# Kernel optimization log

Measured on AMD Instinct MI355X. Metric: run time of the kernel, lower is better.

Reference implementation:

```python
import jax, jax.numpy as jnp
import numpy as np

S_LEN = 256   # seq_len
B = 512       # batch
STATE = 32    # state_dim
ZD = 64       # z_dim
RNN = 512     # rnn_dim
HD = 512      # h_dim
LOG2PI = float(np.log(2.0 * np.pi))


def setup_inputs() -> dict:
    key = jax.random.key(0)
    ks = jax.random.split(key, 12)

    def mat(k, shape, fan_in):
        return jax.random.normal(k, shape, dtype=jnp.float32) * (1.0 / np.sqrt(fan_in))

    z32 = lambda *s: jnp.zeros(s, jnp.float32)
    return {
        "states": jax.random.normal(ks[0], (S_LEN, B, STATE), jnp.float32),
        "z": jax.random.normal(ks[1], (B, ZD), jnp.float32),
        # GRU layer 0: input = concat(state, action) -> 2*STATE
        "Wih0": mat(ks[2], (3 * RNN, 2 * STATE), 2 * STATE),
        "Whh0": mat(ks[3], (3 * RNN, RNN), RNN),
        "bih0": z32(3 * RNN),
        "bhh0": z32(3 * RNN),
        # GRU layer 1: input = hidden of layer 0
        "Wih1": mat(ks[4], (3 * RNN, RNN), RNN),
        "Whh1": mat(ks[5], (3 * RNN, RNN), RNN),
        "bih1": z32(3 * RNN),
        "bhh1": z32(3 * RNN),
        # dec_action_fc: Linear(STATE+ZD+RNN -> HD), ReLU, Linear(HD -> HD), ReLU
        "Wfc1": mat(ks[6], (HD, STATE + ZD + RNN), STATE + ZD + RNN),
        "bfc1": z32(HD),
        "Wfc2": mat(ks[7], (HD, HD), HD),
        "bfc2": z32(HD),
        "Wmean": mat(ks[8], (STATE, HD), HD),
        "bmean": z32(STATE),
        "Wlv": mat(ks[9], (STATE, HD), HD),
        "blv": z32(STATE),
    }


def _gru_step(x, h, Wih, Whh, bih, bhh):
    # PyTorch GRUCell math
    gi = x @ Wih.T + bih  # [B, 3R]
    gh = h @ Whh.T + bhh
    ir, iz, inn = jnp.split(gi, 3, axis=1)
    hr, hz, hn = jnp.split(gh, 3, axis=1)
    r = jax.nn.sigmoid(ir + hr)
    zg = jax.nn.sigmoid(iz + hz)
    n = jnp.tanh(inn + r * hn)
    return (1.0 - zg) * n + zg * h


def reference(states, z, Wih0, Whh0, bih0, bhh0, Wih1, Whh1, bih1, bhh1,
              Wfc1, bfc1, Wfc2, bfc2, Wmean, bmean, Wlv, blv):
    # actions[t] = states[t+1] - states[t]
    actions = states[1:] - states[:-1]
    # loop runs for actions.size(0)-1 = T-2 steps using (states[t], actions[t])
    xs = (states[:-2], actions[:-1])
    Bb = z.shape[0]
    R = Whh0.shape[1]
    h_init = jnp.zeros((2, Bb, R), states.dtype)
    nll_init = jnp.zeros((Bb, states.shape[-1]), states.dtype)

    def step(carry, xt):
        h, nll = carry
        s, a = xt  # [B, STATE] each
        # decode_action: cat(state, z, hidden[-1]) -> MLP -> mean, logvar
        fc_in = jnp.concatenate([s, z, h[1]], axis=1)
        dh = jax.nn.relu(fc_in @ Wfc1.T + bfc1)
        dh = jax.nn.relu(dh @ Wfc2.T + bfc2)
        mean = dh @ Wmean.T + bmean
        logvar = dh @ Wlv.T + blv
        # nll -= Normal(mean, logvar).log_prob(action), std = exp(0.5*logvar)
        nll_t = 0.5 * ((a - mean) ** 2 * jnp.exp(-logvar) + logvar + LOG2PI)
        # update_hidden_state with cat(state, action) through 2-layer GRU
        x_in = jnp.concatenate([s, a], axis=1)
        h0n = _gru_step(x_in, h[0], Wih0, Whh0, bih0, bhh0)
        h1n = _gru_step(h0n, h[1], Wih1, Whh1, bih1, bhh1)
        return (jnp.stack([h0n, h1n]), nll + nll_t), None

    (h, nll), _ = jax.lax.scan(step, (h_init, nll_init), xs)
    return nll  # accumulated NLL, shape [B, STATE]
```

## Files before the change

### kernel.cpp

```cpp
#include <hip/hip_runtime.h>
#include <math.h>

#define BATCH 512
#define LOG2PI 1.8378770664093453f

typedef __attribute__((ext_vector_type(8))) short bfrag;
typedef __attribute__((ext_vector_type(4))) float f32x4;
typedef __attribute__((ext_vector_type(4))) unsigned int u32x4;

#define MFMA(a,b,c) __builtin_amdgcn_mfma_f32_16x16x32_bf16(a,b,c,0,0,0)
#define ASTORE(p,v) __hip_atomic_store((p),(v),__ATOMIC_RELAXED,__HIP_MEMORY_SCOPE_AGENT)
#define ALOAD(p)    __hip_atomic_load((p),__ATOMIC_RELAXED,__HIP_MEMORY_SCOPE_AGENT)

__device__ __forceinline__ void st16_sc1(void* p, u32x4 v){
  asm volatile("global_store_dwordx4 %0, %1, off sc1" :: "v"(p), "v"(v) : "memory");
}

__device__ __forceinline__ float sigm(float x){ return 1.0f/(1.0f+__expf(-x)); }
__device__ __forceinline__ unsigned short f2bf(float f){
  unsigned int u = __builtin_bit_cast(unsigned int, f);
  u += 0x7FFFu + ((u>>16)&1u);
  return (unsigned short)(u>>16);
}
__device__ __forceinline__ bfrag cvt8(const float* __restrict__ p){
  bfrag v;
  #pragma unroll
  for (int e=0;e<8;++e) v[e] = (short)f2bf(p[e]);
  return v;
}
__device__ __forceinline__ bfrag cvt8d(const float* __restrict__ p1, const float* __restrict__ p0){
  bfrag v;
  #pragma unroll
  for (int e=0;e<8;++e) v[e] = (short)f2bf(p1[e]-p0[e]);
  return v;
}

struct Params {
  const float *states, *zin;
  const float *Wih0, *Whh0, *bih0, *bhh0;
  const float *Wih1, *Whh1, *bih1, *bhh1;
  const float *Wfc1, *bfc1, *Wfc2, *bfc2;
  const float *Wmean, *bmean, *Wlv, *blv;
  unsigned short *h0x0, *h0x1, *h0x2;
  unsigned short *h1x0, *h1x1, *h1x2;
  unsigned short *d1x0, *d1x1, *d1x2;
  unsigned short *d2x0, *d2x1, *d2x2;
  float *out;
};

__global__ __launch_bounds__(256, 1) void fused(Params P, unsigned* flags) {
  __shared__ unsigned short sm[74752];
  const int tid  = threadIdx.x;
  const int lane = tid & 63;
  const int wv   = tid >> 6;
  const int r16  = lane & 15, kg = lane >> 4;
  const int blk  = blockIdx.x;
  const int xg   = blk & 7, sub = blk >> 3;

  unsigned short* h0b[3]  = {P.h0x0, P.h0x1, P.h0x2};
  unsigned short* h1b[3]  = {P.h1x0, P.h1x1, P.h1x2};
  unsigned short* dh1b[3] = {P.d1x0, P.d1x1, P.d1x2};
  unsigned short* dh2b[3] = {P.d2x0, P.d2x1, P.d2x2};

  if (xg < 4) {
    const int jt = sub;
    const float* Wsrc[2] = {P.Wih1, P.Whh1};
    #pragma unroll
    for (int m = 0; m < 2; ++m) {
      const float* W = Wsrc[m];
      for (int c = tid; c < 3072; c += 256) {
        int g = c >> 10, rem = c & 1023;
        int r = rem >> 6, k = (rem & 63) << 3;
        *(bfrag*)&sm[(g*16+r)*1032 + m*512 + k] =
          cvt8(&W[((size_t)(g*512 + jt*16 + r))*512 + k]);
      }
    }
  } else if (xg < 6) {
    const int jt = sub;
    for (int c = tid; c < 384; c += 256) {
      int g = c >> 7, rem = c & 127;
      int r = rem >> 3, k = (rem & 7) << 3;
      *(bfrag*)&sm[(g*16+r)*584 + k] =
        cvt8(&P.Wih0[((size_t)(g*512 + jt*16 + r))*64 + k]);
    }
    for (int c = tid; c < 3072; c += 256) {
      int g = c >> 10, rem = c & 1023;
      int r = rem >> 6, k = (rem & 63) << 3;
      *(bfrag*)&sm[(g*16+r)*584 + 64 + k] =
        cvt8(&P.Whh0[((size_t)(g*512 + jt*16 + r))*512 + k]);
    }
  } else if (xg == 6) {
    const int bn = (sub & 7) * 64;
    const int bmB = (sub >> 3) * 128;
    for (int c = tid; c < 4864; c += 256) {
      int n = c / 76, k = (c % 76) << 3;
      *(bfrag*)&sm[n*616 + k] = cvt8(&P.Wfc1[(size_t)(bn + n)*608 + k]);
    }
    for (int c = tid; c < 1024; c += 256) {
      int r = c >> 3, k = (c & 7) << 3;
      *(bfrag*)&sm[47616 + r*64 + k] = cvt8(&P.zin[(size_t)(bmB + r)*64 + k]);
    }
  } else {
    const int bn = (sub & 7) * 64;
    for (int c = tid; c < 4096; c += 256) {
      int n = c >> 6, k = (c & 63) << 3;
      *(bfrag*)&sm[n*520 + k] = cvt8(&P.Wfc2[(size_t)(bn + n)*512 + k]);
    }
    for (int c = tid; c < 4096; c += 256) {
      int m = c >> 6, k = (c & 63) << 3;
      const float* src = (m < 32) ? &P.Wmean[(size_t)m*512 + k]
                                  : &P.Wlv[(size_t)(m-32)*512 + k];
      *(bfrag*)&sm[33280 + m*520 + k] = cvt8(src);
    }
  }

  float b0 = 0.f, b1 = 0.f, b2 = 0.f, b3 = 0.f;
  if (xg < 4) {
    int j = sub*16 + r16;
    b0 = P.bih1[j] + P.bhh1[j];
    b1 = P.bih1[j+512] + P.bhh1[j+512];
    b2 = P.bih1[j+1024]; b3 = P.bhh1[j+1024];
  } else if (xg < 6) {
    int j = sub*16 + r16;
    b0 = P.bih0[j] + P.bhh0[j];
    b1 = P.bih0[j+512] + P.bhh0[j+512];
    b2 = P.bih0[j+1024]; b3 = P.bhh0[j+1024];
  } else if (xg == 6) {
    int nn0 = (sub & 7)*64 + (wv&1)*32 + r16;
    b0 = P.bfc1[nn0]; b1 = P.bfc1[nn0+16];
  } else {
    int nn0 = (sub & 7)*64 + (wv&1)*32 + r16;
    b0 = P.bfc2[nn0]; b1 = P.bfc2[nn0+16];
    int c = wv*16 + r16;
    b2 = (c < 32) ? P.bmean[c] : P.blv[c-32];
  }
  float hs[4][4] = {};
  float nacc0 = 0.f, nacc1 = 0.f;

  for (int u = 0; u <= 256; ++u) {
    if (wv == 0) {
      int pb1 = -1, pb2 = -1;
      const unsigned t1 = (unsigned)u, t2 = (unsigned)(u - 1);
      if (xg >= 4 && xg < 6) {
        if (u >= 1 && lane < 32) pb1 = lane*8 + xg;
        if (u >= 2)              pb2 = (lane>>1)*8 + 2*(xg-4) + (lane&1);
      } else if (xg < 4) {
        if (u >= 1) pb1 = (lane < 32) ? lane*8 + xg : (lane-32)*8 + 4 + (xg>>1);
        if (u >= 2 && lane < 8) pb2 = (xg*8 + lane)*8 + 6;
      } else if (xg == 6) {
        if (u >= 1 && lane < 32) pb1 = lane*8 + (sub>>3);
        if (u >= 2 && lane < 8)  pb2 = ((sub & ~7) + lane)*8 + 7;
      } else {
        if (u >= 1 && lane < 16) pb1 = ((sub & ~7) + (lane&7))*8 + ((lane<8)?6:7);
      }
      unsigned spin = 0;
      while (true) {
        bool ok = true;
        if (pb1 >= 0) ok &= (ALOAD(&flags[pb1*16]) >= t1);
        if (pb2 >= 0) ok &= (ALOAD(&flags[pb2*16]) >= t2);
        if (__all(ok)) break;
        if (++spin > (1u<<26)) break;
        __builtin_amdgcn_s_sleep(1);
      }
    }
    __syncthreads();
    if (tid < 64) __builtin_amdgcn_fence(__ATOMIC_ACQUIRE, "agent");
    __syncthreads();

    const int iu   = u % 3;
    const int ium1 = (u+2) % 3;
    const int ium2 = (u+1) % 3;

    if (xg < 4) {
      if (u >= 1 && u <= 254) {
        const int jt = sub, bmB = xg * 128;
        const unsigned short* h0r = h0b[ium1];
        const unsigned short* h1r = h1b[ium2];
        f32x4 R[2]={}, Z[2]={}, NI[2]={}, NH[2]={};
        const int row0 = bmB + wv*32 + r16;
        #pragma unroll
        for (int half = 0; half < 2; ++half) {
          const unsigned short* asrc = half ? h1r : h0r;
          #pragma unroll 4
          for (int kt = 0; kt < 16; ++kt) {
            const int kk = kt*32 + kg*8;
            const int kl = half*512 + kk;
            bfrag a0 = *(const bfrag*)&asrc[(size_t)row0*512 + kk];
            bfrag a1 = *(const bfrag*)&asrc[(size_t)(row0+16)*512 + kk];
            bfrag bR = *(const bfrag*)&sm[(0*16+r16)*1032 + kl];
            bfrag bZ = *(const bfrag*)&sm[(1*16+r16)*1032 + kl];
            bfrag bN = *(const bfrag*)&sm[(2*16+r16)*1032 + kl];
            R[0]=MFMA(a0,bR,R[0]); R[1]=MFMA(a1,bR,R[1]);
            Z[0]=MFMA(a0,bZ,Z[0]); Z[1]=MFMA(a1,bZ,Z[1]);
            if (!half) { NI[0]=MFMA(a0,bN,NI[0]); NI[1]=MFMA(a1,bN,NI[1]); }
            else       { NH[0]=MFMA(a0,bN,NH[0]); NH[1]=MFMA(a1,bN,NH[1]); }
          }
        }
        unsigned short* exch = sm + 49536;
        #pragma unroll
        for (int fm = 0; fm < 2; ++fm)
          #pragma unroll
          for (int e = 0; e < 4; ++e) {
            int rl = wv*32 + fm*16 + kg*4 + e;
            float r  = sigm(R[fm][e] + b0);
            float zg = sigm(Z[fm][e] + b1);
            float nn = tanhf(NI[fm][e] + b2 + r*(NH[fm][e] + b3));
            float hn = (1.f - zg)*nn + zg*hs[fm][e];
            hs[fm][e] = hn;
            exch[rl*16 + r16] = f2bf(hn);
          }
        __syncthreads();
        {
          unsigned short* dst = h1b[ium1];
          int r = tid >> 1, hc = tid & 1;
          u32x4 v = *(const u32x4*)&exch[r*16 + hc*8];
          st16_sc1(dst + ((size_t)(bmB + r))*512 + jt*16 + hc*8, v);
        }
      }
    } else if (xg < 6) {
      if (u <= 253) {
        const int jt = sub, bmB = (xg - 4) * 256;
        const unsigned short* h0r = h0b[ium1];
        const float* s0 = P.states + (size_t)u*BATCH*32;
        f32x4 R[4]={}, Z[4]={}, NI[4]={}, NH[4]={};
        #pragma unroll
        for (int ks = 0; ks < 2; ++ks) {
          const int kl = ks*32 + kg*8;
          bfrag a[4];
          #pragma unroll
          for (int fm = 0; fm < 4; ++fm) {
            int row = bmB + wv*64 + fm*16 + r16;
            a[fm] = (ks == 0)
              ? cvt8(&s0[(size_t)row*32 + kg*8])
              : cvt8d(&s0[(size_t)(BATCH + row)*32 + kg*8], &s0[(size_t)row*32 + kg*8]);
          }
          bfrag bR = *(const bfrag*)&sm[(0*16+r16)*584 + kl];
          bfrag bZ = *(const bfrag*)&sm[(1*16+r16)*584 + kl];
          bfrag bN = *(const bfrag*)&sm[(2*16+r16)*584 + kl];
          #pragma unroll
          for (int fm = 0; fm < 4; ++fm) {
            R[fm]=MFMA(a[fm],bR,R[fm]); Z[fm]=MFMA(a[fm],bZ,Z[fm]); NI[fm]=MFMA(a[fm],bN,NI[fm]);
          }
        }
        #pragma unroll 2
        for (int kt = 0; kt < 16; ++kt) {
          const int kk = kt*32 + kg*8;
          const int kl = 64 + kk;
          bfrag a[4];
          #pragma unroll
          for (int fm = 0; fm < 4; ++fm) {
            int row = bmB + wv*64 + fm*16 + r16;
            a[fm] = *(const bfrag*)&h0r[(size_t)row*512 + kk];
          }
          bfrag bR = *(const bfrag*)&sm[(0*16+r16)*584 + kl];
          bfrag bZ = *(const bfrag*)&sm[(1*16+r16)*584 + kl];
          bfrag bN = *(const bfrag*)&sm[(2*16+r16)*584 + kl];
          #pragma unroll
          for (int fm = 0; fm < 4; ++fm) {
            R[fm]=MFMA(a[fm],bR,R[fm]); Z[fm]=MFMA(a[fm],bZ,Z[fm]); NH[fm]=MFMA(a[fm],bN,NH[fm]);
          }
        }
        unsigned short* exch = sm + 28032;
        #pragma unroll
        for (int fm = 0; fm < 4; ++fm)
          #pragma unroll
          for (int e = 0; e < 4; ++e) {
            int rl = wv*64 + fm*16 + kg*4 + e;
            float r  = sigm(R[fm][e] + b0);
            float zg = sigm(Z[fm][e] + b1);
            float nn = tanhf(NI[fm][e] + b2 + r*(NH[fm][e] + b3));
            float hn = (1.f - zg)*nn + zg*hs[fm][e];
            hs[fm][e] = hn;
            exch[rl*16 + r16] = f2bf(hn);
          }
        __syncthreads();
        {
          unsigned short* dst = h0b[iu];
          int r = tid;
          u32x4 v0 = *(const u32x4*)&exch[r*16];
          u32x4 v1 = *(const u32x4*)&exch[r*16 + 8];
          unsigned short* dp = dst + ((size_t)(bmB + r))*512 + jt*16;
          st16_sc1(dp,     v0);
          st16_sc1(dp + 8, v1);
        }
      }
    } else if (xg == 6) {
      if (u >= 1 && u <= 254) {
        const int bmB = (sub >> 3) * 128, bnB = (sub & 7) * 64;
        const unsigned short* h1r = h1b[ium2];
        const float* s0 = P.states + (size_t)(u-1)*BATCH*32;
        f32x4 acc[4][2] = {};
        const int arow = bmB + (wv>>1)*64;
        const int bcol = (wv&1)*32;
        #pragma unroll 2
        for (int kt = 0; kt < 19; ++kt) {
          const int k = kt*32 + kg*8;
          bfrag a[4];
          #pragma unroll
          for (int fm = 0; fm < 4; ++fm) {
            int row = arow + fm*16 + r16;
            int rl  = row - bmB;
            if (kt == 0)      a[fm] = cvt8(&s0[(size_t)row*32 + k]);
            else if (kt <= 2) a[fm] = *(const bfrag*)&sm[47616 + rl*64 + (k - 32)];
            else              a[fm] = *(const bfrag*)&h1r[(size_t)row*512 + (k - 96)];
          }
          bfrag bf0 = *(const bfrag*)&sm[(bcol      + r16)*616 + k];
          bfrag bf1 = *(const bfrag*)&sm[(bcol + 16 + r16)*616 + k];
          #pragma unroll
          for (int fm = 0; fm < 4; ++fm) {
            acc[fm][0] = MFMA(a[fm], bf0, acc[fm][0]);
            acc[fm][1] = MFMA(a[fm], bf1, acc[fm][1]);
          }
        }
        unsigned short* exch = sm + 39424;
        #pragma unroll
        for (int fm = 0; fm < 4; ++fm)
          #pragma unroll
          for (int fn = 0; fn < 2; ++fn) {
            float bias = fn ? b1 : b0;
            #pragma unroll
            for (int e = 0; e < 4; ++e) {
              int rl = (wv>>1)*64 + fm*16 + kg*4 + e;
              int cl = bcol + fn*16 + r16;
              exch[rl*64 + cl] = f2bf(fmaxf(acc[fm][fn][e] + bias, 0.f));
            }
          }
        __syncthreads();
        {
          unsigned short* dst = dh1b[ium1];
          int r = tid >> 1, hc = tid & 1;
          #pragma unroll
          for (int q = 0; q < 4; ++q) {
            u32x4 v = *(const u32x4*)&exch[r*64 + hc*32 + q*8];
            st16_sc1(dst + ((size_t)(bmB + r))*512 + bnB + hc*32 + q*8, v);
          }
        }
        __syncthreads();
      }
    } else {
      if (u >= 2 && u <= 255) {
        const int bmB = (sub >> 3) * 128, bnB = (sub & 7) * 64;
        const unsigned short* dr = dh1b[ium2];
        f32x4 acc[4][2] = {};
        const int arow = bmB + (wv>>1)*64;
        const int bcol = (wv&1)*32;
        #pragma unroll 2
        for (int kt = 0; kt < 16; ++kt) {
          const int k = kt*32 + kg*8;
          bfrag a[4];
          #pragma unroll
          for (int fm = 0; fm < 4; ++fm) {
            int row = arow + fm*16 + r16;
            a[fm] = *(const bfrag*)&dr[(size_t)row*512 + k];
          }
          bfrag bf0 = *(const bfrag*)&sm[(bcol      + r16)*520 + k];
          bfrag bf1 = *(const bfrag*)&sm[(bcol + 16 + r16)*520 + k];
          #pragma unroll
          for (int fm = 0; fm < 4; ++fm) {
            acc[fm][0] = MFMA(a[fm], bf0, acc[fm][0]);
            acc[fm][1] = MFMA(a[fm], bf1, acc[fm][1]);
          }
        }
        unsigned short* exch = sm + 66560;
        #pragma unroll
        for (int fm = 0; fm < 4; ++fm)
          #pragma unroll
          for (int fn = 0; fn < 2; ++fn) {
            float bias = fn ? b1 : b0;
            #pragma unroll
            for (int e = 0; e < 4; ++e) {
              int rl = (wv>>1)*64 + fm*16 + kg*4 + e;
              int cl = bcol + fn*16 + r16;
              exch[rl*64 + cl] = f2bf(fmaxf(acc[fm][fn][e] + bias, 0.f));
            }
          }
        __syncthreads();
        {
          unsigned short* dst = dh2b[ium2];
          int r = tid >> 1, hc = tid & 1;
          #pragma unroll
          for (int q = 0; q < 4; ++q) {
            u32x4 v = *(const u32x4*)&exch[r*64 + hc*32 + q*8];
            st16_sc1(dst + ((size_t)(bmB + r))*512 + bnB + hc*32 + q*8, v);
          }
        }
      }
      if (u >= 3) {
        const int t = u - 3;
        const unsigned short* dr = dh2b[iu];
        f32x4 acc = {};
        #pragma unroll 2
        for (int kt = 0; kt < 16; ++kt) {
          const int k = kt*32 + kg*8;
          bfrag a = *(const bfrag*)&dr[(size_t)(sub*16 + r16)*512 + k];
          bfrag b = *(const bfrag*)&sm[33280 + (wv*16 + r16)*520 + k];
          acc = MFMA(a, b, acc);
        }
        __syncthreads();
        float* exch = (float*)(sm + 66560);
        const int c = wv*16 + r16;
        #pragma unroll
        for (int e = 0; e < 4; ++e)
          exch[(kg*4+e)*66 + c] = acc[e] + b2;
        __syncthreads();
        const float* s0 = P.states + (size_t)t*BATCH*32;
        #pragma unroll
        for (int e2 = 0; e2 < 2; ++e2) {
          int idx = tid*2 + e2;
          int r = idx >> 5, i = idx & 31;
          int b = sub*16 + r;
          float mean = exch[r*66 + i], lv = exch[r*66 + 32 + i];
          float av = s0[(size_t)(BATCH + b)*32 + i] - s0[(size_t)b*32 + i];
          float d = av - mean;
          float v = 0.5f*(d*d*__expf(-lv) + lv + LOG2PI);
          if (e2) nacc1 += v; else nacc0 += v;
        }
      }
    }

    __syncthreads();
    if (tid == 0) ASTORE(&flags[blk*16], (unsigned)(u+1));
  }

  if (xg == 7) {
    #pragma unroll
    for (int e2 = 0; e2 < 2; ++e2) {
      int idx = tid*2 + e2;
      int b = sub*16 + (idx >> 5), i = idx & 31;
      P.out[(size_t)b*32 + i] = e2 ? nacc1 : nacc0;
    }
  }
}

extern "C" void kernel_launch(void* const* d_in, const int* in_sizes, int n_in,
                              void* d_out, int out_size, void* d_ws, size_t ws_size,
                              hipStream_t stream) {
  Params P;
  P.states = (const float*)d_in[0];
  P.zin    = (const float*)d_in[1];
  P.Wih0   = (const float*)d_in[2];
  P.Whh0   = (const float*)d_in[3];
  P.bih0   = (const float*)d_in[4];
  P.bhh0   = (const float*)d_in[5];
  P.Wih1   = (const float*)d_in[6];
  P.Whh1   = (const float*)d_in[7];
  P.bih1   = (const float*)d_in[8];
  P.bhh1   = (const float*)d_in[9];
  P.Wfc1   = (const float*)d_in[10];
  P.bfc1   = (const float*)d_in[11];
  P.Wfc2   = (const float*)d_in[12];
  P.bfc2   = (const float*)d_in[13];
  P.Wmean  = (const float*)d_in[14];
  P.bmean  = (const float*)d_in[15];
  P.Wlv    = (const float*)d_in[16];
  P.blv    = (const float*)d_in[17];
  P.out = (float*)d_out;

  const size_t HB = (size_t)512*512;
  unsigned short* u = (unsigned short*)d_ws;
  P.h0x0 = u;        P.h0x1 = u + HB;   P.h0x2 = u + 2*HB;
  P.h1x0 = u + 3*HB; P.h1x1 = u + 4*HB; P.h1x2 = u + 5*HB;
  P.d1x0 = u + 6*HB; P.d1x1 = u + 7*HB; P.d1x2 = u + 8*HB;
  P.d2x0 = u + 9*HB; P.d2x1 = u + 10*HB; P.d2x2 = u + 11*HB;
  unsigned* flags = (unsigned*)(u + 12*HB);

  hipMemsetAsync(u, 0, 6*HB*sizeof(unsigned short), stream);
  hipMemsetAsync(flags, 0, 256*16*sizeof(unsigned), stream);
  hipMemsetAsync(d_out, 0, (size_t)out_size*sizeof(float), stream);

  fused<<<dim3(256), dim3(256), 0, stream>>>(P, flags);
}
```

Before: 4.368 ms.

## Software-pipeline global activation loads with volatile register ring buffers, drop acquire fence

Each per-step GEMM stage now preloads several k-slices of the inter-block activations (h0, h1, dh1, dh2) into a register ring buffer and refills it ahead of use, so global load latency overlaps with MFMA work. Loads go through volatile 16-byte reads, which bypass stale caching and take the place of the explicit agent-scope acquire fence and its extra barrier after the flag spin. This cuts per-step latency in the serial recurrence. In exchange it raises register pressure and relies on volatile loads alone for memory ordering against the relaxed flag reads, which may be weaker than the removed fence.

```diff
diff --git a/kernel.cpp b/kernel.cpp
--- a/kernel.cpp
+++ b/kernel.cpp
@@ -14,6 +14,10 @@
 
 __device__ __forceinline__ void st16_sc1(void* p, u32x4 v){
   asm volatile("global_store_dwordx4 %0, %1, off sc1" :: "v"(p), "v"(v) : "memory");
+}
+__device__ __forceinline__ bfrag vld16(const unsigned short* p){
+  u32x4 v = *(const volatile u32x4*)p;
+  union { u32x4 u; bfrag b; } c; c.u = v; return c.b;
 }
 
 __device__ __forceinline__ float sigm(float x){ return 1.0f/(1.0f+__expf(-x)); }
@@ -164,8 +168,6 @@
       }
     }
     __syncthreads();
-    if (tid < 64) __builtin_amdgcn_fence(__ATOMIC_ACQUIRE, "agent");
-    __syncthreads();
 
     const int iu   = u % 3;
     const int ium1 = (u+2) % 3;
@@ -178,23 +180,30 @@
         const unsigned short* h1r = h1b[ium2];
         f32x4 R[2]={}, Z[2]={}, NI[2]={}, NH[2]={};
         const int row0 = bmB + wv*32 + r16;
-        #pragma unroll
-        for (int half = 0; half < 2; ++half) {
-          const unsigned short* asrc = half ? h1r : h0r;
-          #pragma unroll 4
-          for (int kt = 0; kt < 16; ++kt) {
-            const int kk = kt*32 + kg*8;
-            const int kl = half*512 + kk;
-            bfrag a0 = *(const bfrag*)&asrc[(size_t)row0*512 + kk];
-            bfrag a1 = *(const bfrag*)&asrc[(size_t)(row0+16)*512 + kk];
-            bfrag bR = *(const bfrag*)&sm[(0*16+r16)*1032 + kl];
-            bfrag bZ = *(const bfrag*)&sm[(1*16+r16)*1032 + kl];
-            bfrag bN = *(const bfrag*)&sm[(2*16+r16)*1032 + kl];
-            R[0]=MFMA(a0,bR,R[0]); R[1]=MFMA(a1,bR,R[1]);
-            Z[0]=MFMA(a0,bZ,Z[0]); Z[1]=MFMA(a1,bZ,Z[1]);
-            if (!half) { NI[0]=MFMA(a0,bN,NI[0]); NI[1]=MFMA(a1,bN,NI[1]); }
-            else       { NH[0]=MFMA(a0,bN,NH[0]); NH[1]=MFMA(a1,bN,NH[1]); }
-          }
+        const unsigned short* pA = h0r + (size_t)row0*512 + kg*8;
+        const unsigned short* pB = pA + 16*512;
+        const unsigned short* qA = h1r + (size_t)row0*512 + kg*8;
+        const unsigned short* qB = qA + 16*512;
+        bfrag s0[8], s1[8];
+        #pragma unroll
+        for (int p = 0; p < 8; ++p) { s0[p]=vld16(pA+p*32); s1[p]=vld16(pB+p*32); }
+        #pragma unroll
+        for (int q = 0; q < 32; ++q) {
+          const int slot = q & 7;
+          bfrag a0 = s0[slot], a1 = s1[slot];
+          if (q + 8 < 32) {
+            const int n = q + 8;
+            if (n < 16) { s0[slot]=vld16(pA+n*32);      s1[slot]=vld16(pB+n*32); }
+            else        { s0[slot]=vld16(qA+(n-16)*32); s1[slot]=vld16(qB+(n-16)*32); }
+          }
+          const int kl = (q < 16 ? q*32 : 512 + (q-16)*32) + kg*8;
+          bfrag bR = *(const bfrag*)&sm[(0*16+r16)*1032 + kl];
+          bfrag bZ = *(const bfrag*)&sm[(1*16+r16)*1032 + kl];
+          bfrag bN = *(const bfrag*)&sm[(2*16+r16)*1032 + kl];
+          R[0]=MFMA(a0,bR,R[0]); R[1]=MFMA(a1,bR,R[1]);
+          Z[0]=MFMA(a0,bZ,Z[0]); Z[1]=MFMA(a1,bZ,Z[1]);
+          if (q < 16) { NI[0]=MFMA(a0,bN,NI[0]); NI[1]=MFMA(a1,bN,NI[1]); }
+          else        { NH[0]=MFMA(a0,bN,NH[0]); NH[1]=MFMA(a1,bN,NH[1]); }
         }
         unsigned short* exch = sm + 49536;
         #pragma unroll
@@ -221,8 +230,14 @@
       if (u <= 253) {
         const int jt = sub, bmB = (xg - 4) * 256;
         const unsigned short* h0r = h0b[ium1];
-        const float* s0 = P.states + (size_t)u*BATCH*32;
+        const float* s0p = P.states + (size_t)u*BATCH*32;
         f32x4 R[4]={}, Z[4]={}, NI[4]={}, NH[4]={};
+        bfrag st[4][4];
+        #pragma unroll
+        for (int p = 0; p < 4; ++p)
+          #pragma unroll
+          for (int fm = 0; fm < 4; ++fm)
+            st[p][fm] = vld16(h0r + (size_t)(bmB + wv*64 + fm*16 + r16)*512 + p*32 + kg*8);
         #pragma unroll
         for (int ks = 0; ks < 2; ++ks) {
           const int kl = ks*32 + kg*8;
@@ -231,8 +246,8 @@
           for (int fm = 0; fm < 4; ++fm) {
             int row = bmB + wv*64 + fm*16 + r16;
             a[fm] = (ks == 0)
-              ? cvt8(&s0[(size_t)row*32 + kg*8])
-              : cvt8d(&s0[(size_t)(BATCH + row)*32 + kg*8], &s0[(size_t)row*32 + kg*8]);
+              ? cvt8(&s0p[(size_t)row*32 + kg*8])
+              : cvt8d(&s0p[(size_t)(BATCH + row)*32 + kg*8], &s0p[(size_t)row*32 + kg*8]);
           }
           bfrag bR = *(const bfrag*)&sm[(0*16+r16)*584 + kl];
           bfrag bZ = *(const bfrag*)&sm[(1*16+r16)*584 + kl];
@@ -242,16 +257,17 @@
             R[fm]=MFMA(a[fm],bR,R[fm]); Z[fm]=MFMA(a[fm],bZ,Z[fm]); NI[fm]=MFMA(a[fm],bN,NI[fm]);
           }
         }
-        #pragma unroll 2
+        #pragma unroll
         for (int kt = 0; kt < 16; ++kt) {
-          const int kk = kt*32 + kg*8;
-          const int kl = 64 + kk;
+          const int slot = kt & 3;
           bfrag a[4];
           #pragma unroll
           for (int fm = 0; fm < 4; ++fm) {
-            int row = bmB + wv*64 + fm*16 + r16;
-            a[fm] = *(const bfrag*)&h0r[(size_t)row*512 + kk];
-          }
+            a[fm] = st[slot][fm];
+            if (kt + 4 < 16)
+              st[slot][fm] = vld16(h0r + (size_t)(bmB + wv*64 + fm*16 + r16)*512 + (kt+4)*32 + kg*8);
+          }
+          const int kl = 64 + kt*32 + kg*8;
           bfrag bR = *(const bfrag*)&sm[(0*16+r16)*584 + kl];
           bfrag bZ = *(const bfrag*)&sm[(1*16+r16)*584 + kl];
           bfrag bN = *(const bfrag*)&sm[(2*16+r16)*584 + kl];
@@ -288,22 +304,46 @@
       if (u >= 1 && u <= 254) {
         const int bmB = (sub >> 3) * 128, bnB = (sub & 7) * 64;
         const unsigned short* h1r = h1b[ium2];
-        const float* s0 = P.states + (size_t)(u-1)*BATCH*32;
+        const float* s0p = P.states + (size_t)(u-1)*BATCH*32;
         f32x4 acc[4][2] = {};
         const int arow = bmB + (wv>>1)*64;
         const int bcol = (wv&1)*32;
-        #pragma unroll 2
-        for (int kt = 0; kt < 19; ++kt) {
+        bfrag st[4][4];
+        #pragma unroll
+        for (int p = 0; p < 4; ++p)
+          #pragma unroll
+          for (int fm = 0; fm < 4; ++fm)
+            st[p][fm] = vld16(h1r + (size_t)(arow + fm*16 + r16)*512 + p*32 + kg*8);
+        #pragma unroll
+        for (int kt = 0; kt < 3; ++kt) {
           const int k = kt*32 + kg*8;
           bfrag a[4];
           #pragma unroll
           for (int fm = 0; fm < 4; ++fm) {
             int row = arow + fm*16 + r16;
             int rl  = row - bmB;
-            if (kt == 0)      a[fm] = cvt8(&s0[(size_t)row*32 + k]);
-            else if (kt <= 2) a[fm] = *(const bfrag*)&sm[47616 + rl*64 + (k - 32)];
-            else              a[fm] = *(const bfrag*)&h1r[(size_t)row*512 + (k - 96)];
-          }
+            if (kt == 0) a[fm] = cvt8(&s0p[(size_t)row*32 + k]);
+            else         a[fm] = *(const bfrag*)&sm[47616 + rl*64 + (k - 32)];
+          }
+          bfrag bf0 = *(const bfrag*)&sm[(bcol      + r16)*616 + k];
+          bfrag bf1 = *(const bfrag*)&sm[(bcol + 16 + r16)*616 + k];
+          #pragma unroll
+          for (int fm = 0; fm < 4; ++fm) {
+            acc[fm][0] = MFMA(a[fm], bf0, acc[fm][0]);
+            acc[fm][1] = MFMA(a[fm], bf1, acc[fm][1]);
+          }
+        }
+        #pragma unroll
+        for (int ck = 0; ck < 16; ++ck) {
+          const int slot = ck & 3;
+          bfrag a[4];
+          #pragma unroll
+          for (int fm = 0; fm < 4; ++fm) {
+            a[fm] = st[slot][fm];
+            if (ck + 4 < 16)
+              st[slot][fm] = vld16(h1r + (size_t)(arow + fm*16 + r16)*512 + (ck+4)*32 + kg*8);
+          }
+          const int k = 96 + ck*32 + kg*8;
           bfrag bf0 = *(const bfrag*)&sm[(bcol      + r16)*616 + k];
           bfrag bf1 = *(const bfrag*)&sm[(bcol + 16 + r16)*616 + k];
           #pragma unroll
@@ -344,15 +384,23 @@
         f32x4 acc[4][2] = {};
         const int arow = bmB + (wv>>1)*64;
         const int bcol = (wv&1)*32;
-        #pragma unroll 2
+        bfrag st[4][4];
+        #pragma unroll
+        for (int p = 0; p < 4; ++p)
+          #pragma unroll
+          for (int fm = 0; fm < 4; ++fm)
+            st[p][fm] = vld16(dr + (size_t)(arow + fm*16 + r16)*512 + p*32 + kg*8);
+        #pragma unroll
         for (int kt = 0; kt < 16; ++kt) {
+          const int slot = kt & 3;
+          bfrag a[4];
+          #pragma unroll
+          for (int fm = 0; fm < 4; ++fm) {
+            a[fm] = st[slot][fm];
+            if (kt + 4 < 16)
+              st[slot][fm] = vld16(dr + (size_t)(arow + fm*16 + r16)*512 + (kt+4)*32 + kg*8);
+          }
           const int k = kt*32 + kg*8;
-          bfrag a[4];
-          #pragma unroll
-          for (int fm = 0; fm < 4; ++fm) {
-            int row = arow + fm*16 + r16;
-            a[fm] = *(const bfrag*)&dr[(size_t)row*512 + k];
-          }
           bfrag bf0 = *(const bfrag*)&sm[(bcol      + r16)*520 + k];
           bfrag bf1 = *(const bfrag*)&sm[(bcol + 16 + r16)*520 + k];
           #pragma unroll
@@ -389,11 +437,16 @@
         const int t = u - 3;
         const unsigned short* dr = dh2b[iu];
         f32x4 acc = {};
-        #pragma unroll 2
+        const unsigned short* hp = dr + (size_t)(sub*16 + r16)*512 + kg*8;
+        bfrag hs8[8];
+        #pragma unroll
+        for (int p = 0; p < 8; ++p) hs8[p] = vld16(hp + p*32);
+        #pragma unroll
         for (int kt = 0; kt < 16; ++kt) {
-          const int k = kt*32 + kg*8;
-          bfrag a = *(const bfrag*)&dr[(size_t)(sub*16 + r16)*512 + k];
-          bfrag b = *(const bfrag*)&sm[33280 + (wv*16 + r16)*520 + k];
+          const int slot = kt & 7;
+          bfrag a = hs8[slot];
+          if (kt + 8 < 16) hs8[slot] = vld16(hp + (kt+8)*32);
+          bfrag b = *(const bfrag*)&sm[33280 + (wv*16 + r16)*520 + kt*32 + kg*8];
           acc = MFMA(a, b, acc);
         }
         __syncthreads();
@@ -403,14 +456,14 @@
         for (int e = 0; e < 4; ++e)
           exch[(kg*4+e)*66 + c] = acc[e] + b2;
         __syncthreads();
-        const float* s0 = P.states + (size_t)t*BATCH*32;
+        const float* s0p = P.states + (size_t)t*BATCH*32;
         #pragma unroll
         for (int e2 = 0; e2 < 2; ++e2) {
           int idx = tid*2 + e2;
           int r = idx >> 5, i = idx & 31;
           int b = sub*16 + r;
           float mean = exch[r*66 + i], lv = exch[r*66 + 32 + i];
-          float av = s0[(size_t)(BATCH + b)*32 + i] - s0[(size_t)b*32 + i];
+          float av = s0p[(size_t)(BATCH + b)*32 + i] - s0p[(size_t)b*32 + i];
           float d = av - mean;
           float v = 0.5f*(d*d*__expf(-lv) + lv + LOG2PI);
           if (e2) nacc1 += v; else nacc0 += v;
```

Result: slower. 5.821 ms (+33.3%).

## Deepen activation ring buffers to eight slots and relax WAR flag waits

Applied to the files above, without the earlier changes.

Replaces the triple-buffered activation arrays with an 8-deep ring indexed by step modulo 8. The write-after-read dependency waits now check consumers from six steps back instead of one, so producer blocks can run further ahead of consumers. This takes the anti-dependency stalls out of the per-step critical path. The cost is more workspace memory and a larger memset, and buffer reuse now depends on the deeper slack being correct.

```diff
diff --git a/kernel.cpp b/kernel.cpp
--- a/kernel.cpp
+++ b/kernel.cpp
@@ -3,6 +3,7 @@
 
 #define BATCH 512
 #define LOG2PI 1.8378770664093453f
+#define HB 262144
 
 typedef __attribute__((ext_vector_type(8))) short bfrag;
 typedef __attribute__((ext_vector_type(4))) float f32x4;
@@ -41,10 +42,7 @@
   const float *Wih1, *Whh1, *bih1, *bhh1;
   const float *Wfc1, *bfc1, *Wfc2, *bfc2;
   const float *Wmean, *bmean, *Wlv, *blv;
-  unsigned short *h0x0, *h0x1, *h0x2;
-  unsigned short *h1x0, *h1x1, *h1x2;
-  unsigned short *d1x0, *d1x1, *d1x2;
-  unsigned short *d2x0, *d2x1, *d2x2;
+  unsigned short *act;
   float *out;
 };
 
@@ -57,10 +55,10 @@
   const int blk  = blockIdx.x;
   const int xg   = blk & 7, sub = blk >> 3;
 
-  unsigned short* h0b[3]  = {P.h0x0, P.h0x1, P.h0x2};
-  unsigned short* h1b[3]  = {P.h1x0, P.h1x1, P.h1x2};
-  unsigned short* dh1b[3] = {P.d1x0, P.d1x1, P.d1x2};
-  unsigned short* dh2b[3] = {P.d2x0, P.d2x1, P.d2x2};
+  unsigned short* h0 = P.act;
+  unsigned short* h1 = P.act +  8*(size_t)HB;
+  unsigned short* d1 = P.act + 16*(size_t)HB;
+  unsigned short* d2 = P.act + 24*(size_t)HB;
 
   if (xg < 4) {
     const int jt = sub;
@@ -140,16 +138,16 @@
   for (int u = 0; u <= 256; ++u) {
     if (wv == 0) {
       int pb1 = -1, pb2 = -1;
-      const unsigned t1 = (unsigned)u, t2 = (unsigned)(u - 1);
+      const unsigned t1 = (unsigned)u, t2 = (unsigned)(u - 6);
       if (xg >= 4 && xg < 6) {
         if (u >= 1 && lane < 32) pb1 = lane*8 + xg;
-        if (u >= 2)              pb2 = (lane>>1)*8 + 2*(xg-4) + (lane&1);
+        if (u >= 7)              pb2 = (lane>>1)*8 + 2*(xg-4) + (lane&1);
       } else if (xg < 4) {
         if (u >= 1) pb1 = (lane < 32) ? lane*8 + xg : (lane-32)*8 + 4 + (xg>>1);
-        if (u >= 2 && lane < 8) pb2 = (xg*8 + lane)*8 + 6;
+        if (u >= 7 && lane < 8) pb2 = (xg*8 + lane)*8 + 6;
       } else if (xg == 6) {
         if (u >= 1 && lane < 32) pb1 = lane*8 + (sub>>3);
-        if (u >= 2 && lane < 8)  pb2 = ((sub & ~7) + lane)*8 + 7;
+        if (u >= 7 && lane < 8)  pb2 = ((sub & ~7) + lane)*8 + 7;
       } else {
         if (u >= 1 && lane < 16) pb1 = ((sub & ~7) + (lane&7))*8 + ((lane<8)?6:7);
       }
@@ -167,15 +165,16 @@
     if (tid < 64) __builtin_amdgcn_fence(__ATOMIC_ACQUIRE, "agent");
     __syncthreads();
 
-    const int iu   = u % 3;
-    const int ium1 = (u+2) % 3;
-    const int ium2 = (u+1) % 3;
+    const int ju  = u & 7;
+    const int jm1 = (u+7) & 7;
+    const int jm2 = (u+6) & 7;
+    const int jm3 = (u+5) & 7;
 
     if (xg < 4) {
       if (u >= 1 && u <= 254) {
         const int jt = sub, bmB = xg * 128;
-        const unsigned short* h0r = h0b[ium1];
-        const unsigned short* h1r = h1b[ium2];
+        const unsigned short* h0r = h0 + (size_t)jm1*HB;
+        const unsigned short* h1r = h1 + (size_t)jm2*HB;
         f32x4 R[2]={}, Z[2]={}, NI[2]={}, NH[2]={};
         const int row0 = bmB + wv*32 + r16;
         #pragma unroll
@@ -211,7 +210,7 @@
           }
         __syncthreads();
         {
-          unsigned short* dst = h1b[ium1];
+          unsigned short* dst = h1 + (size_t)jm1*HB;
           int r = tid >> 1, hc = tid & 1;
           u32x4 v = *(const u32x4*)&exch[r*16 + hc*8];
           st16_sc1(dst + ((size_t)(bmB + r))*512 + jt*16 + hc*8, v);
@@ -220,8 +219,8 @@
     } else if (xg < 6) {
       if (u <= 253) {
         const int jt = sub, bmB = (xg - 4) * 256;
-        const unsigned short* h0r = h0b[ium1];
-        const float* s0 = P.states + (size_t)u*BATCH*32;
+        const unsigned short* h0r = h0 + (size_t)jm1*HB;
+        const float* s0p = P.states + (size_t)u*BATCH*32;
         f32x4 R[4]={}, Z[4]={}, NI[4]={}, NH[4]={};
         #pragma unroll
         for (int ks = 0; ks < 2; ++ks) {
@@ -231,8 +230,8 @@
           for (int fm = 0; fm < 4; ++fm) {
             int row = bmB + wv*64 + fm*16 + r16;
             a[fm] = (ks == 0)
-              ? cvt8(&s0[(size_t)row*32 + kg*8])
-              : cvt8d(&s0[(size_t)(BATCH + row)*32 + kg*8], &s0[(size_t)row*32 + kg*8]);
+              ? cvt8(&s0p[(size_t)row*32 + kg*8])
+              : cvt8d(&s0p[(size_t)(BATCH + row)*32 + kg*8], &s0p[(size_t)row*32 + kg*8]);
           }
           bfrag bR = *(const bfrag*)&sm[(0*16+r16)*584 + kl];
           bfrag bZ = *(const bfrag*)&sm[(1*16+r16)*584 + kl];
@@ -275,7 +274,7 @@
           }
         __syncthreads();
         {
-          unsigned short* dst = h0b[iu];
+          unsigned short* dst = h0 + (size_t)ju*HB;
           int r = tid;
           u32x4 v0 = *(const u32x4*)&exch[r*16];
           u32x4 v1 = *(const u32x4*)&exch[r*16 + 8];
@@ -287,8 +286,8 @@
     } else if (xg == 6) {
       if (u >= 1 && u <= 254) {
         const int bmB = (sub >> 3) * 128, bnB = (sub & 7) * 64;
-        const unsigned short* h1r = h1b[ium2];
-        const float* s0 = P.states + (size_t)(u-1)*BATCH*32;
+        const unsigned short* h1r = h1 + (size_t)jm2*HB;
+        const float* s0p = P.states + (size_t)(u-1)*BATCH*32;
         f32x4 acc[4][2] = {};
         const int arow = bmB + (wv>>1)*64;
         const int bcol = (wv&1)*32;
@@ -300,7 +299,7 @@
           for (int fm = 0; fm < 4; ++fm) {
             int row = arow + fm*16 + r16;
             int rl  = row - bmB;
-            if (kt == 0)      a[fm] = cvt8(&s0[(size_t)row*32 + k]);
+            if (kt == 0)      a[fm] = cvt8(&s0p[(size_t)row*32 + k]);
             else if (kt <= 2) a[fm] = *(const bfrag*)&sm[47616 + rl*64 + (k - 32)];
             else              a[fm] = *(const bfrag*)&h1r[(size_t)row*512 + (k - 96)];
           }
@@ -327,7 +326,7 @@
           }
         __syncthreads();
         {
-          unsigned short* dst = dh1b[ium1];
+          unsigned short* dst = d1 + (size_t)jm1*HB;
           int r = tid >> 1, hc = tid & 1;
           #pragma unroll
           for (int q = 0; q < 4; ++q) {
@@ -340,7 +339,7 @@
     } else {
       if (u >= 2 && u <= 255) {
         const int bmB = (sub >> 3) * 128, bnB = (sub & 7) * 64;
-        const unsigned short* dr = dh1b[ium2];
+        const unsigned short* dr = d1 + (size_t)jm2*HB;
         f32x4 acc[4][2] = {};
         const int arow = bmB + (wv>>1)*64;
         const int bcol = (wv&1)*32;
@@ -376,7 +375,7 @@
           }
         __syncthreads();
         {
-          unsigned short* dst = dh2b[ium2];
+          unsigned short* dst = d2 + (size_t)jm2*HB;
           int r = tid >> 1, hc = tid & 1;
           #pragma unroll
           for (int q = 0; q < 4; ++q) {
@@ -387,7 +386,7 @@
       }
       if (u >= 3) {
         const int t = u - 3;
-        const unsigned short* dr = dh2b[iu];
+        const unsigned short* dr = d2 + (size_t)jm3*HB;
         f32x4 acc = {};
         #pragma unroll 2
         for (int kt = 0; kt < 16; ++kt) {
@@ -403,14 +402,14 @@
         for (int e = 0; e < 4; ++e)
           exch[(kg*4+e)*66 + c] = acc[e] + b2;
         __syncthreads();
-        const float* s0 = P.states + (size_t)t*BATCH*32;
+        const float* s0p = P.states + (size_t)t*BATCH*32;
         #pragma unroll
         for (int e2 = 0; e2 < 2; ++e2) {
           int idx = tid*2 + e2;
           int r = idx >> 5, i = idx & 31;
           int b = sub*16 + r;
           float mean = exch[r*66 + i], lv = exch[r*66 + 32 + i];
-          float av = s0[(size_t)(BATCH + b)*32 + i] - s0[(size_t)b*32 + i];
+          float av = s0p[(size_t)(BATCH + b)*32 + i] - s0p[(size_t)b*32 + i];
           float d = av - mean;
           float v = 0.5f*(d*d*__expf(-lv) + lv + LOG2PI);
           if (e2) nacc1 += v; else nacc0 += v;
@@ -455,16 +454,11 @@
   P.Wlv    = (const float*)d_in[16];
   P.blv    = (const float*)d_in[17];
   P.out = (float*)d_out;
-
-  const size_t HB = (size_t)512*512;
-  unsigned short* u = (unsigned short*)d_ws;
-  P.h0x0 = u;        P.h0x1 = u + HB;   P.h0x2 = u + 2*HB;
-  P.h1x0 = u + 3*HB; P.h1x1 = u + 4*HB; P.h1x2 = u + 5*HB;
-  P.d1x0 = u + 6*HB; P.d1x1 = u + 7*HB; P.d1x2 = u + 8*HB;
-  P.d2x0 = u + 9*HB; P.d2x1 = u + 10*HB; P.d2x2 = u + 11*HB;
-  unsigned* flags = (unsigned*)(u + 12*HB);
-
-  hipMemsetAsync(u, 0, 6*HB*sizeof(unsigned short), stream);
+  P.act = (unsigned short*)d_ws;
+
+  unsigned* flags = (unsigned*)(P.act + 32*(size_t)HB);
+
+  hipMemsetAsync(P.act, 0, 16*(size_t)HB*sizeof(unsigned short), stream);
   hipMemsetAsync(flags, 0, 256*16*sizeof(unsigned), stream);
   hipMemsetAsync(d_out, 0, (size_t)out_size*sizeof(float), stream);
 
```

Result: no change. 4.339 ms (-0.7%).
